# Performance work log

Hardware: AMD Instinct MI355X
Metric: run time of the kernel (lower is better)

The kernel has to match this reference:

```python
import jax, jax.numpy as jnp
import numpy as np

N, C, E, Q, H, NC = 50000, 128, 1600000, 500000, 256, 2
BN_EPS = 1e-5


def gru_step(x, h, wih, whh, bih, bhh):
    # single-step torch.nn.GRU, gate order (r, z, n); x,h: [C, C] rows as batch
    gi = x @ wih.T + bih
    gh = h @ whh.T + bhh
    ir, iz, inn = jnp.split(gi, 3, axis=-1)
    hr, hz, hn = jnp.split(gh, 3, axis=-1)
    r = jax.nn.sigmoid(ir + hr)
    z = jax.nn.sigmoid(iz + hz)
    n = jnp.tanh(inn + r * hn)
    return (1.0 - z) * n + z * h


def gcn_conv(x, w, src, dst, ew):
    # GCNConv with fixed weight w and symmetric gcn_norm incl. self-loops
    xw = x @ w
    deg = jnp.zeros((N,), xw.dtype).at[dst].add(ew) + 1.0  # +1 self-loop
    dinv = jax.lax.rsqrt(deg)
    norm = dinv[src] * ew * dinv[dst]
    out = jnp.zeros_like(xw).at[dst].add(xw[src] * norm[:, None])
    return out + xw * (dinv * dinv)[:, None]  # self-loop contribution


def evolve_gcno(x, src, dst, ew, w_init, wih, whh, bih, bhh):
    w = gru_step(w_init, w_init, wih, whh, bih, bhh)
    return gcn_conv(x, w, src, dst, ew)


def setup_inputs():
    key = jax.random.key(0)
    ks = jax.random.split(key, 40)
    inp = {}
    inp["X"] = jax.random.normal(ks[0], (N, C), jnp.float32)
    inp["edge_index"] = jax.random.randint(ks[1], (2, E), 0, N, jnp.int32)
    inp["edge_weight"] = jax.random.uniform(ks[2], (E,), jnp.float32)
    inp["edge1"] = jax.random.randint(ks[3], (Q,), 0, N, jnp.int32)
    inp["edge2"] = jax.random.randint(ks[4], (Q,), 0, N, jnp.int32)
    s = 1.0 / np.sqrt(C)
    i = 5
    for l in range(2):
        inp[f"w{l}_init"] = jax.random.uniform(ks[i], (C, C), jnp.float32, -s, s); i += 1
        inp[f"w{l}_ih"] = jax.random.uniform(ks[i], (3 * C, C), jnp.float32, -s, s); i += 1
        inp[f"w{l}_hh"] = jax.random.uniform(ks[i], (3 * C, C), jnp.float32, -s, s); i += 1
        inp[f"b{l}_ih"] = jax.random.uniform(ks[i], (3 * C,), jnp.float32, -s, s); i += 1
        inp[f"b{l}_hh"] = jax.random.uniform(ks[i], (3 * C,), jnp.float32, -s, s); i += 1
    dims = [(H, C), (H, H), (NC, H)]
    for l, (o, fi) in enumerate(dims):
        sl = 1.0 / np.sqrt(fi)
        inp[f"lin_w{l}"] = jax.random.uniform(ks[i], (o, fi), jnp.float32, -sl, sl); i += 1
        inp[f"lin_b{l}"] = jax.random.uniform(ks[i], (o,), jnp.float32, -sl, sl); i += 1
    for l in range(2):
        inp[f"bn_g{l}"] = jax.random.uniform(ks[i], (H,), jnp.float32, 0.5, 1.5); i += 1
        inp[f"bn_b{l}"] = 0.1 * jax.random.normal(ks[i], (H,), jnp.float32); i += 1
        inp[f"bn_m{l}"] = 0.1 * jax.random.normal(ks[i], (H,), jnp.float32); i += 1
        inp[f"bn_v{l}"] = jax.random.uniform(ks[i], (H,), jnp.float32, 0.5, 1.5); i += 1
    return inp


def reference(X, edge_index, edge_weight, edge1, edge2,
              w0_init, w0_ih, w0_hh, b0_ih, b0_hh,
              w1_init, w1_ih, w1_hh, b1_ih, b1_hh,
              lin_w0, lin_b0, lin_w1, lin_b1, lin_w2, lin_b2,
              bn_g0, bn_b0, bn_m0, bn_v0, bn_g1, bn_b1, bn_m1, bn_v1):
    src, dst = edge_index[0], edge_index[1]
    # EGCNO: two EvolveGCNO layers + relu (dropout is identity in eval)
    x = jax.nn.relu(evolve_gcno(X, src, dst, edge_weight, w0_init, w0_ih, w0_hh, b0_ih, b0_hh))
    x = jax.nn.relu(evolve_gcno(x, src, dst, edge_weight, w1_init, w1_ih, w1_hh, b1_ih, b1_hh))
    # edge pair gather + hadamard
    h = x[edge1] * x[edge2]  # [Q, C]
    bn = [(bn_g0, bn_b0, bn_m0, bn_v0), (bn_g1, bn_b1, bn_m1, bn_v1)]
    lins = [(lin_w0, lin_b0), (lin_w1, lin_b1)]
    for (w, b), (g, bb, m, v) in zip(lins, bn):
        h = h @ w.T + b
        h = g * (h - m) * jax.lax.rsqrt(v + BN_EPS) + bb  # BatchNorm1d (eval)
        h = jax.nn.relu(h)
    h = h @ lin_w2.T + lin_b2
    return jax.nn.log_softmax(h, axis=-1)
```

## Files before the change

### kernel.cpp

```cpp
#include <hip/hip_runtime.h>
#include <math.h>

#define N_NODES 50000
#define C_DIM   128
#define E_EDGES 1600000
#define Q_PAIRS 500000
#define H_DIM   256
#define N_CLS   2
#define BN_EPS  1e-5f

typedef __attribute__((ext_vector_type(8))) short bf16x8;
typedef __attribute__((ext_vector_type(4))) short s16x4;
typedef __attribute__((ext_vector_type(4))) unsigned short u16x4;
typedef __attribute__((ext_vector_type(4))) float f32x4;

#define VMCNT0 asm volatile("s_waitcnt vmcnt(0)" ::: "memory")
#define VMCNT1 asm volatile("s_waitcnt vmcnt(1)" ::: "memory")
#define VMCNT2 asm volatile("s_waitcnt vmcnt(2)" ::: "memory")
#define SBAR do { __builtin_amdgcn_s_barrier(); \
                  __builtin_amdgcn_sched_barrier(0); } while (0)

#define DEG_SCALE 2097152.0f

__device__ __forceinline__ unsigned short f2bf(float x) {
    unsigned u = __float_as_uint(x);
    u += 0x7fffu + ((u >> 16) & 1u);
    return (unsigned short)(u >> 16);
}
__device__ __forceinline__ float bf2f(unsigned short h) {
    return __uint_as_float(((unsigned)h) << 16);
}

__global__ __launch_bounds__(256) void k_init(unsigned long long* dpack, int* qcnt) {
    int i = blockIdx.x * 256 + threadIdx.x;
    if (i < N_NODES) { dpack[i] = 0ULL; qcnt[i] = 0; }
}
__global__ __launch_bounds__(256) void k_deg_hist(const int* __restrict__ dst,
                                                  const float* __restrict__ ew,
                                                  unsigned long long* dpack) {
    int e = blockIdx.x * 256 + threadIdx.x;
    if (e < E_EDGES) {
        unsigned pv = __float2uint_rn(ew[e] * DEG_SCALE);
        atomicAdd(&dpack[dst[e]], (1ULL << 32) | (unsigned long long)pv);
    }
}
__global__ __launch_bounds__(256) void k_qhist(const int* __restrict__ e1, int* qcnt) {
    int q = blockIdx.x * 256 + threadIdx.x;
    if (q < Q_PAIRS) atomicAdd(&qcnt[e1[q]], 1);
}

__global__ __launch_bounds__(1024) void k_scan1(const int* __restrict__ cnt, int stride,
                                                int* __restrict__ locincl,
                                                int* __restrict__ bsum) {
    __shared__ int pa[1024], pb[1024];
    int t = threadIdx.x;
    int x = blockIdx.x * 1024 + t;
    int v = (x < N_NODES) ? cnt[(size_t)x * stride] : 0;
    pa[t] = v;
    __syncthreads();
    int* sp = pa; int* dp = pb;
    for (int o = 1; o < 1024; o <<= 1) {
        int u = sp[t] + ((t >= o) ? sp[t - o] : 0);
        dp[t] = u;
        __syncthreads();
        int* tmp = sp; sp = dp; dp = tmp;
    }
    if (x < N_NODES) locincl[x] = sp[t];
    if (t == 1023) bsum[blockIdx.x] = sp[1023];
}
__global__ __launch_bounds__(64) void k_scan2(const int* __restrict__ bsum,
                                              int* __restrict__ boff) {
    int t = threadIdx.x;
    int v = (t < 49) ? bsum[t] : 0;
    int own = v;
    for (int o = 1; o < 64; o <<= 1) {
        int u = __shfl_up(v, o, 64);
        if (t >= o) v += u;
    }
    if (t < 49) boff[t] = v - own;
}
__global__ __launch_bounds__(1024) void k_scan3(const int* __restrict__ cnt, int stride,
                                                int* __restrict__ pos,
                                                const int* __restrict__ boff,
                                                int* __restrict__ off,
                                                const unsigned long long* __restrict__ dpack,
                                                float* __restrict__ dinv) {
    int x = blockIdx.x * 1024 + threadIdx.x;
    if (x >= N_NODES) return;
    int incl = pos[x];
    int c = cnt[(size_t)x * stride];
    int o = boff[blockIdx.x] + incl - c;
    off[x] = o;
    pos[x] = o;
    if (x == N_NODES - 1) off[N_NODES] = o + c;
    if (dpack) {
        unsigned lo = (unsigned)(dpack[x] & 0xffffffffULL);
        dinv[x] = rsqrtf(1.0f + (float)lo * (1.0f / DEG_SCALE));
    }
}

__global__ __launch_bounds__(256) void k_fill(const int* __restrict__ src,
                                              const int* __restrict__ dst,
                                              const float* __restrict__ ew,
                                              const float* __restrict__ dinv,
                                              int* pos,
                                              int2* __restrict__ csr) {
    int e = blockIdx.x * 256 + threadIdx.x;
    if (e >= E_EDGES) return;
    int s = src[e], d = dst[e];
    int slot = atomicAdd(&pos[d], 1);
    int2 p;
    p.x = s;
    p.y = __float_as_int(dinv[s] * ew[e] * dinv[d]);
    csr[slot] = p;
}
__global__ __launch_bounds__(256) void k_qfill(const int* __restrict__ e1,
                                               const int* __restrict__ e2,
                                               int* qpos,
                                               int2* __restrict__ qpair,
                                               int* __restrict__ qidx) {
    int q = blockIdx.x * 256 + threadIdx.x;
    if (q >= Q_PAIRS) return;
    int a = e1[q];
    int slot = atomicAdd(&qpos[a], 1);
    int2 p; p.x = a; p.y = e2[q];
    qpair[slot] = p;
    qidx[slot] = q;
}

__global__ __launch_bounds__(128) void k_gru2(
    const float* __restrict__ wi0, const float* __restrict__ wih0, const float* __restrict__ whh0,
    const float* __restrict__ bih0, const float* __restrict__ bhh0, float* __restrict__ we0,
    const float* __restrict__ wi1, const float* __restrict__ wih1, const float* __restrict__ whh1,
    const float* __restrict__ bih1, const float* __restrict__ bhh1, float* __restrict__ we1) {
    __shared__ float xrow[C_DIM];
    int layer = blockIdx.x >> 7;
    int i = blockIdx.x & 127, j = threadIdx.x;
    const float* w_init = layer ? wi1 : wi0;
    const float* wih = layer ? wih1 : wih0;
    const float* whh = layer ? whh1 : whh0;
    const float* bih = layer ? bih1 : bih0;
    const float* bhh = layer ? bhh1 : bhh0;
    float* w_out = layer ? we1 : we0;
    xrow[j] = w_init[i * C_DIM + j];
    __syncthreads();
    float gi[3], gh[3];
#pragma unroll
    for (int g = 0; g < 3; ++g) {
        const float* wi = wih + (size_t)(g * C_DIM + j) * C_DIM;
        const float* wh = whh + (size_t)(g * C_DIM + j) * C_DIM;
        float ai = 0.f, ah = 0.f;
        for (int k = 0; k < C_DIM; ++k) { ai += xrow[k] * wi[k]; ah += xrow[k] * wh[k]; }
        gi[g] = ai + bih[g * C_DIM + j];
        gh[g] = ah + bhh[g * C_DIM + j];
    }
    float r = 1.f / (1.f + expf(-(gi[0] + gh[0])));
    float z = 1.f / (1.f + expf(-(gi[1] + gh[1])));
    float n = tanhf(gi[2] + r * gh[2]);
    w_out[i * C_DIM + j] = (1.f - z) * n + z * xrow[j];
}

__global__ __launch_bounds__(256) void k_xbf(const float* __restrict__ x,
                                             unsigned short* __restrict__ xb) {
    int i = (blockIdx.x * 256 + threadIdx.x) * 8;
    f32x4 a = *(const f32x4*)(x + i);
    f32x4 b = *(const f32x4*)(x + i + 4);
    bf16x8 o;
#pragma unroll
    for (int e = 0; e < 4; ++e) { o[e] = (short)f2bf(a[e]); o[e + 4] = (short)f2bf(b[e]); }
    *(bf16x8*)(xb + i) = o;
}

__global__ __launch_bounds__(256) void k_agg(const unsigned short* __restrict__ xb,
                                             const float* __restrict__ dinv,
                                             const int* __restrict__ off,
                                             const int2* __restrict__ csr,
                                             float* __restrict__ agg) {
    int tid = blockIdx.x * 256 + threadIdx.x;
    int n = tid >> 5;
    int c = (tid & 31) << 2;
    float dv = dinv[n];
    float d2 = dv * dv;
    u16x4 xs = *(const u16x4*)(xb + (size_t)n * C_DIM + c);
    float4 acc;
    acc.x = d2 * bf2f(xs[0]); acc.y = d2 * bf2f(xs[1]);
    acc.z = d2 * bf2f(xs[2]); acc.w = d2 * bf2f(xs[3]);
    int i = off[n], e = off[n + 1];
    for (; i + 8 <= e; i += 8) {
        int2 q0 = csr[i], q1 = csr[i + 1], q2 = csr[i + 2], q3 = csr[i + 3];
        int2 q4 = csr[i + 4], q5 = csr[i + 5], q6 = csr[i + 6], q7 = csr[i + 7];
        u16x4 v0 = *(const u16x4*)(xb + (size_t)q0.x * C_DIM + c);
        u16x4 v1 = *(const u16x4*)(xb + (size_t)q1.x * C_DIM + c);
        u16x4 v2 = *(const u16x4*)(xb + (size_t)q2.x * C_DIM + c);
        u16x4 v3 = *(const u16x4*)(xb + (size_t)q3.x * C_DIM + c);
        u16x4 v4 = *(const u16x4*)(xb + (size_t)q4.x * C_DIM + c);
        u16x4 v5 = *(const u16x4*)(xb + (size_t)q5.x * C_DIM + c);
        u16x4 v6 = *(const u16x4*)(xb + (size_t)q6.x * C_DIM + c);
        u16x4 v7 = *(const u16x4*)(xb + (size_t)q7.x * C_DIM + c);
        float w0 = __int_as_float(q0.y), w1 = __int_as_float(q1.y);
        float w2 = __int_as_float(q2.y), w3 = __int_as_float(q3.y);
        float w4 = __int_as_float(q4.y), w5 = __int_as_float(q5.y);
        float w6 = __int_as_float(q6.y), w7 = __int_as_float(q7.y);
        acc.x += w0 * bf2f(v0[0]) + w1 * bf2f(v1[0]) + w2 * bf2f(v2[0]) + w3 * bf2f(v3[0])
               + w4 * bf2f(v4[0]) + w5 * bf2f(v5[0]) + w6 * bf2f(v6[0]) + w7 * bf2f(v7[0]);
        acc.y += w0 * bf2f(v0[1]) + w1 * bf2f(v1[1]) + w2 * bf2f(v2[1]) + w3 * bf2f(v3[1])
               + w4 * bf2f(v4[1]) + w5 * bf2f(v5[1]) + w6 * bf2f(v6[1]) + w7 * bf2f(v7[1]);
        acc.z += w0 * bf2f(v0[2]) + w1 * bf2f(v1[2]) + w2 * bf2f(v2[2]) + w3 * bf2f(v3[2])
               + w4 * bf2f(v4[2]) + w5 * bf2f(v5[2]) + w6 * bf2f(v6[2]) + w7 * bf2f(v7[2]);
        acc.w += w0 * bf2f(v0[3]) + w1 * bf2f(v1[3]) + w2 * bf2f(v2[3]) + w3 * bf2f(v3[3])
               + w4 * bf2f(v4[3]) + w5 * bf2f(v5[3]) + w6 * bf2f(v6[3]) + w7 * bf2f(v7[3]);
    }
    for (; i < e; ++i) {
        int2 pe = csr[i];
        float w = __int_as_float(pe.y);
        u16x4 v = *(const u16x4*)(xb + (size_t)pe.x * C_DIM + c);
        acc.x += w * bf2f(v[0]); acc.y += w * bf2f(v[1]);
        acc.z += w * bf2f(v[2]); acc.w += w * bf2f(v[3]);
    }
    *(float4*)(agg + (size_t)n * C_DIM + c) = acc;
}

__global__ __launch_bounds__(256) void k_prep_w(const float* __restrict__ w,
                                                const float* __restrict__ g,
                                                const float* __restrict__ v,
                                                int kdim, int total,
                                                unsigned short* __restrict__ outp) {
    int idx = blockIdx.x * 256 + threadIdx.x;
    if (idx >= total) return;
    int e = idx & 7, col = (idx >> 3) & 255, kg = (idx >> 11) & 3;
    int kb = idx >> 13;
    int k = kb * 32 + kg * 8 + e;
    float sc = g[col] * rsqrtf(v[col] + BN_EPS);
    outp[idx] = f2bf(w[(size_t)col * kdim + k] * sc);
}
__global__ __launch_bounds__(256) void k_prep_conv(const float* __restrict__ we0,
                                                   const float* __restrict__ we1,
                                                   unsigned short* __restrict__ Wc0,
                                                   unsigned short* __restrict__ Wc1) {
    int idx = blockIdx.x * 256 + threadIdx.x;
    int e = idx & 7, col = (idx >> 3) & 127, kg = (idx >> 10) & 3;
    int plane = (idx >> 12) & 1, kb = (idx >> 13) & 3, layer = idx >> 15;
    int k = kb * 32 + kg * 8 + e;
    const float* we = layer ? we1 : we0;
    float x = we[(size_t)k * C_DIM + col];
    unsigned short hi = f2bf(x);
    unsigned short o = plane ? f2bf(x - bf2f(hi)) : hi;
    (layer ? Wc1 : Wc0)[idx & 32767] = o;
}

__global__ __launch_bounds__(512) void k_prep_shift(
    const float* __restrict__ lb0, const float* __restrict__ bg0, const float* __restrict__ bb0,
    const float* __restrict__ bm0, const float* __restrict__ bv0,
    const float* __restrict__ lb1, const float* __restrict__ bg1, const float* __restrict__ bb1,
    const float* __restrict__ bm1, const float* __restrict__ bv1,
    float* __restrict__ shift0, float* __restrict__ shift1) {
    int j = threadIdx.x;
    if (j < 256) {
        float sc = bg0[j] * rsqrtf(bv0[j] + BN_EPS);
        shift0[j] = (lb0[j] - bm0[j]) * sc + bb0[j];
    } else {
        int i = j - 256;
        float sc = bg1[i] * rsqrtf(bv1[i] + BN_EPS);
        shift1[i] = (lb1[i] - bm1[i]) * sc + bb1[i];
    }
}

template <int OUT_BF>
__global__ __launch_bounds__(512) void k_gemm(const float* __restrict__ agg,
                                              const unsigned short* __restrict__ Wc,
                                              float* __restrict__ y,
                                              unsigned short* __restrict__ yb) {
    __shared__ __align__(16) char smem[3 * 8192];
    const int t = threadIdx.x, lane = t & 63, wave = t >> 6;
    const int qg = wave >> 1, ch = wave & 1;
    const int l16 = lane & 15, kg = lane >> 4;
    const int qrow = qg * 16 + l16;
    const int node = blockIdx.x * 64 + qrow;
    const int nodec = node < N_NODES ? node : N_NODES - 1;

    auto STG = [&](int sidx, int b) {
        const char* g = (const char*)Wc + sidx * 8192 + wave * 1024 + lane * 16;
        char* d = smem + b * 8192 + wave * 1024;
        __builtin_amdgcn_global_load_lds((const __attribute__((address_space(1))) void*)g,
                                         (__attribute__((address_space(3))) void*)d, 16, 0, 0);
    };
    STG(0, 0); STG(1, 1);

    bf16x8 bh[4], bl[4];
    const float* ar = agg + (size_t)nodec * C_DIM;
#pragma unroll
    for (int kb = 0; kb < 4; ++kb) {
        int k0 = kb * 32 + kg * 8;
        f32x4 a0 = *(const f32x4*)(ar + k0);
        f32x4 a1 = *(const f32x4*)(ar + k0 + 4);
#pragma unroll
        for (int e = 0; e < 4; ++e) {
            unsigned short h0 = f2bf(a0[e]);
            bh[kb][e] = (short)h0; bl[kb][e] = (short)f2bf(a0[e] - bf2f(h0));
            unsigned short h1 = f2bf(a1[e]);
            bh[kb][e + 4] = (short)h1; bl[kb][e + 4] = (short)f2bf(a1[e] - bf2f(h1));
        }
    }
    f32x4 acc[4];
#pragma unroll
    for (int i = 0; i < 4; ++i) acc[i] = 0.f;

#pragma unroll
    for (int s = 0; s < 8; ++s) {
        if (s < 7) { VMCNT1; } else { VMCNT0; }
        SBAR;
        if (s + 2 < 8) STG(s + 2, (s + 2) % 3);
        const unsigned short* strip = (const unsigned short*)(smem + (s % 3) * 8192);
        const int kb = s >> 1;
        __builtin_amdgcn_s_setprio(1);
#pragma unroll
        for (int jc8 = 0; jc8 < 4; ++jc8) {
            int col = (ch * 4 + jc8) * 16 + l16;
            bf16x8 a = *(const bf16x8*)&strip[kg * 1024 + col * 8];
            acc[jc8] = __builtin_amdgcn_mfma_f32_16x16x32_bf16(a, bh[kb], acc[jc8], 0, 0, 0);
            if ((s & 1) == 0)
                acc[jc8] = __builtin_amdgcn_mfma_f32_16x16x32_bf16(a, bl[kb], acc[jc8], 0, 0, 0);
        }
        __builtin_amdgcn_s_setprio(0);
    }

    if (node < N_NODES) {
#pragma unroll
        for (int jc8 = 0; jc8 < 4; ++jc8) {
            int j0 = (ch * 4 + jc8) * 16 + kg * 4;
            if (OUT_BF) {
                u16x4 v;
#pragma unroll
                for (int r = 0; r < 4; ++r) v[r] = f2bf(fmaxf(acc[jc8][r], 0.f));
                *(u16x4*)(yb + (size_t)node * C_DIM + j0) = v;
            } else {
                float4 v;
                v.x = fmaxf(acc[jc8][0], 0.f); v.y = fmaxf(acc[jc8][1], 0.f);
                v.z = fmaxf(acc[jc8][2], 0.f); v.w = fmaxf(acc[jc8][3], 0.f);
                *(float4*)(y + (size_t)node * C_DIM + j0) = v;
            }
        }
    }
}

__global__ __launch_bounds__(512, 4) void k_mlp(const float* __restrict__ y,
                                             const int2* __restrict__ qpair,
                                             const int* __restrict__ qidx,
                                             const unsigned short* __restrict__ W0p,
                                             const unsigned short* __restrict__ W1p,
                                             const float* __restrict__ shift0,
                                             const float* __restrict__ shift1,
                                             const float* __restrict__ w2,
                                             const float* __restrict__ b2,
                                             float* __restrict__ out) {
    __shared__ __align__(16) char smem[81920];
    unsigned short* l1b = (unsigned short*)(smem + 49152);
    float* red = (float*)smem;

    const int t = threadIdx.x;
    const int lane = t & 63;
    const int wave = t >> 6;
    const int qs = wave >> 2, cg = wave & 3;
    const int l16 = lane & 15, kg = lane >> 4;
    const int qb = blockIdx.x * 64;

    auto STG = [&](const unsigned short* W, int sidx, int b) {
        const char* g = (const char*)W + ((size_t)sidx << 14) + wave * 2048 + lane * 16;
        char* d = smem + b * 16384 + wave * 2048;
        __builtin_amdgcn_global_load_lds((const __attribute__((address_space(1))) void*)g,
                                         (__attribute__((address_space(3))) void*)d, 16, 0, 0);
        __builtin_amdgcn_global_load_lds((const __attribute__((address_space(1))) void*)(g + 1024),
                                         (__attribute__((address_space(3))) void*)(d + 1024), 16, 0, 0);
    };

    STG(W0p, 0, 0); STG(W0p, 1, 1);

    {
        int k2 = lane * 2;
        int G = lane >> 2;
        int off = k2 & 7;
#pragma unroll
        for (int qi = 0; qi < 8; ++qi) {
            int qrow = wave * 8 + qi;
            int q = qb + qrow; if (q >= Q_PAIRS) q = Q_PAIRS - 1;
            int2 pr = qpair[q];
            const float* ya = y + (size_t)pr.x * C_DIM;
            const float* yb = y + (size_t)pr.y * C_DIM;
            float2 a = *(const float2*)(ya + k2);
            float2 b = *(const float2*)(yb + k2);
            int idx = qrow * 256 + ((G ^ (qrow & 7)) << 3) + off;
            l1b[idx] = f2bf(a.x * b.x);
            l1b[idx + 1] = f2bf(a.y * b.y);
        }
    }
    __syncthreads();

    bf16x8 bh[2][4];
#pragma unroll
    for (int qq = 0; qq < 2; ++qq) {
        int qrow = qs * 32 + qq * 16 + l16;
#pragma unroll
        for (int kb = 0; kb < 4; ++kb) {
            int gidx = qrow * 256 + (((kb * 4 + kg) ^ (qrow & 7)) * 8);
            bh[qq][kb] = *(const bf16x8*)&l1b[gidx];
        }
    }

    f32x4 acc[2][4];
#pragma unroll
    for (int qq = 0; qq < 2; ++qq)
#pragma unroll
        for (int jc = 0; jc < 4; ++jc) acc[qq][jc] = 0.f;

#pragma unroll
    for (int s = 0; s < 4; ++s) {
        if (s < 3) { VMCNT2; } else { VMCNT0; }
        SBAR;
        if (s + 2 < 4) STG(W0p, s + 2, (s + 2) % 3);
        const unsigned short* strip = (const unsigned short*)(smem + (s % 3) * 16384);
        __builtin_amdgcn_s_setprio(1);
#pragma unroll
        for (int jc = 0; jc < 4; ++jc) {
            int col = cg * 64 + jc * 16 + l16;
            bf16x8 a = *(const bf16x8*)&strip[kg * 2048 + col * 8];
            acc[0][jc] = __builtin_amdgcn_mfma_f32_16x16x32_bf16(a, bh[0][s], acc[0][jc], 0, 0, 0);
            acc[1][jc] = __builtin_amdgcn_mfma_f32_16x16x32_bf16(a, bh[1][s], acc[1][jc], 0, 0, 0);
        }
        __builtin_amdgcn_s_setprio(0);
    }

#pragma unroll
    for (int qq = 0; qq < 2; ++qq) {
        int qrow = qs * 32 + qq * 16 + l16;
#pragma unroll
        for (int jc = 0; jc < 4; ++jc) {
            int jg = cg * 4 + jc;
            int j0 = jg * 16 + kg * 4;
            f32x4 sh = *(const f32x4*)(shift0 + j0);
            s16x4 th;
#pragma unroll
            for (int r = 0; r < 4; ++r)
                th[r] = (short)f2bf(fmaxf(acc[qq][jc][r] + sh[r], 0.f));
            int G = jg * 2 + (kg >> 1);
            int idx = qrow * 256 + ((G ^ (qrow & 7)) * 8) + (kg & 1) * 4;
            *(s16x4*)&l1b[idx] = th;
        }
    }
    __syncthreads();

    f32x4 acc2[2][4];
#pragma unroll
    for (int qq = 0; qq < 2; ++qq)
#pragma unroll
        for (int jc = 0; jc < 4; ++jc) acc2[qq][jc] = 0.f;
    STG(W1p, 0, 0); STG(W1p, 1, 1);
    bf16x8 bh2[2];
#pragma unroll
    for (int s = 0; s < 8; ++s) {
        if (s < 7) { VMCNT2; } else { VMCNT0; }
        SBAR;
        if (s + 2 < 8) STG(W1p, s + 2, (s + 2) % 3);
        const unsigned short* strip = (const unsigned short*)(smem + (s % 3) * 16384);
#pragma unroll
        for (int qq = 0; qq < 2; ++qq) {
            int qrow = qs * 32 + qq * 16 + l16;
            int gidx = qrow * 256 + (((s * 4 + kg) ^ (qrow & 7)) * 8);
            bh2[qq] = *(const bf16x8*)&l1b[gidx];
        }
        __builtin_amdgcn_s_setprio(1);
#pragma unroll
        for (int jc = 0; jc < 4; ++jc) {
            int col = cg * 64 + jc * 16 + l16;
            bf16x8 a = *(const bf16x8*)&strip[kg * 2048 + col * 8];
            acc2[0][jc] = __builtin_amdgcn_mfma_f32_16x16x32_bf16(a, bh2[0], acc2[0][jc], 0, 0, 0);
            acc2[1][jc] = __builtin_amdgcn_mfma_f32_16x16x32_bf16(a, bh2[1], acc2[1][jc], 0, 0, 0);
        }
        __builtin_amdgcn_s_setprio(0);
    }

    float p[2][2] = {};
#pragma unroll
    for (int qq = 0; qq < 2; ++qq)
#pragma unroll
        for (int jc = 0; jc < 4; ++jc) {
            int j0 = (cg * 4 + jc) * 16 + kg * 4;
            f32x4 sh = *(const f32x4*)(shift1 + j0);
            f32x4 wa = *(const f32x4*)(w2 + j0);
            f32x4 wb = *(const f32x4*)(w2 + H_DIM + j0);
#pragma unroll
            for (int r = 0; r < 4; ++r) {
                float v = fmaxf(acc2[qq][jc][r] + sh[r], 0.f);
                p[qq][0] += v * wa[r];
                p[qq][1] += v * wb[r];
            }
        }
#pragma unroll
    for (int qq = 0; qq < 2; ++qq) {
        p[qq][0] += __shfl_xor(p[qq][0], 16, 64); p[qq][0] += __shfl_xor(p[qq][0], 32, 64);
        p[qq][1] += __shfl_xor(p[qq][1], 16, 64); p[qq][1] += __shfl_xor(p[qq][1], 32, 64);
    }
    __syncthreads();
    if (kg == 0) {
#pragma unroll
        for (int qq = 0; qq < 2; ++qq) {
            int base = ((qs * 2 + qq) * 16 + l16) * 2;
            red[(base + 0) * 4 + cg] = p[qq][0];
            red[(base + 1) * 4 + cg] = p[qq][1];
        }
    }
    __syncthreads();
    if (t < 64) {
        int q = qb + t;
        if (q < Q_PAIRS) {
            int base = t * 2;
            float l0 = red[base * 4 + 0] + red[base * 4 + 1] + red[base * 4 + 2] + red[base * 4 + 3] + b2[0];
            float l1v = red[(base + 1) * 4 + 0] + red[(base + 1) * 4 + 1]
                      + red[(base + 1) * 4 + 2] + red[(base + 1) * 4 + 3] + b2[1];
            float mx = fmaxf(l0, l1v);
            float lse = mx + logf(expf(l0 - mx) + expf(l1v - mx));
            float2 o; o.x = l0 - lse; o.y = l1v - lse;
            *(float2*)(out + (size_t)qidx[q] * N_CLS) = o;
        }
    }
}

extern "C" void kernel_launch(void* const* d_in, const int* in_sizes, int n_in,
                              void* d_out, int out_size, void* d_ws, size_t ws_size,
                              hipStream_t stream) {
    const float* X  = (const float*)d_in[0];
    const int*   ei = (const int*)d_in[1];
    const float* ew = (const float*)d_in[2];
    const int*   e1 = (const int*)d_in[3];
    const int*   e2 = (const int*)d_in[4];
    const float* w_init[2] = {(const float*)d_in[5],  (const float*)d_in[10]};
    const float* w_ih[2]   = {(const float*)d_in[6],  (const float*)d_in[11]};
    const float* w_hh[2]   = {(const float*)d_in[7],  (const float*)d_in[12]};
    const float* b_ih[2]   = {(const float*)d_in[8],  (const float*)d_in[13]};
    const float* b_hh[2]   = {(const float*)d_in[9],  (const float*)d_in[14]};
    const float* lw0 = (const float*)d_in[15]; const float* lb0 = (const float*)d_in[16];
    const float* lw1 = (const float*)d_in[17]; const float* lb1 = (const float*)d_in[18];
    const float* lw2 = (const float*)d_in[19]; const float* lb2 = (const float*)d_in[20];
    const float* bg0 = (const float*)d_in[21]; const float* bb0 = (const float*)d_in[22];
    const float* bm0 = (const float*)d_in[23]; const float* bv0 = (const float*)d_in[24];
    const float* bg1 = (const float*)d_in[25]; const float* bb1 = (const float*)d_in[26];
    const float* bm1 = (const float*)d_in[27]; const float* bv1 = (const float*)d_in[28];
    const int* src = ei;
    const int* dst = ei + E_EDGES;

    char* ws = (char*)d_ws;
    size_t o = 0;
    auto alloc = [&](size_t bytes) { char* p = ws + o; o += (bytes + 63) & ~(size_t)63; return p; };
    float* bufA   = (float*)alloc((size_t)N_NODES * C_DIM * 4);
    float* bufB   = (float*)alloc((size_t)N_NODES * C_DIM * 4);
    unsigned short* xbf = (unsigned short*)alloc((size_t)N_NODES * C_DIM * 2);
    unsigned short* ybf = (unsigned short*)alloc((size_t)N_NODES * C_DIM * 2);
    float* dinv   = (float*)alloc(N_NODES * 4);
    float* we0    = (float*)alloc(C_DIM * C_DIM * 4);
    float* we1    = (float*)alloc(C_DIM * C_DIM * 4);
    float* shift0 = (float*)alloc(H_DIM * 4);
    float* shift1 = (float*)alloc(H_DIM * 4);
    unsigned long long* dpack = (unsigned long long*)alloc((size_t)N_NODES * 8);
    int*   pos    = (int*)alloc(N_NODES * 4);
    int*   off    = (int*)alloc((N_NODES + 1) * 4);
    int*   bsum   = (int*)alloc(64 * 4);
    int*   boff   = (int*)alloc(64 * 4);
    int*   qcnt   = (int*)alloc(N_NODES * 4);
    int*   qpos   = (int*)alloc(N_NODES * 4);
    int*   qoff   = (int*)alloc((N_NODES + 1) * 4);
    int*   qbsum  = (int*)alloc(64 * 4);
    int*   qboff  = (int*)alloc(64 * 4);
    int2*  csr    = (int2*)alloc((size_t)E_EDGES * 8);
    int2*  qpair  = (int2*)alloc((size_t)Q_PAIRS * 8);
    int*   qidx   = (int*)alloc((size_t)Q_PAIRS * 4);
    unsigned short* W0p = (unsigned short*)alloc(32768 * 2);
    unsigned short* W1p = (unsigned short*)alloc(65536 * 2);
    unsigned short* Wc0 = (unsigned short*)alloc(32768 * 2);
    unsigned short* Wc1 = (unsigned short*)alloc(32768 * 2);
    if (o > ws_size) return;

    dim3 b256(256);
    const int gN = (N_NODES + 255) / 256;
    const int gE = (E_EDGES + 255) / 256;
    const int gQ = (Q_PAIRS + 255) / 256;

    k_init<<<gN, b256, 0, stream>>>(dpack, qcnt);
    k_deg_hist<<<gE, b256, 0, stream>>>(dst, ew, dpack);
    k_qhist<<<gQ, b256, 0, stream>>>(e1, qcnt);
    k_scan1<<<49, dim3(1024), 0, stream>>>((const int*)dpack + 1, 2, pos, bsum);
    k_scan2<<<1, dim3(64), 0, stream>>>(bsum, boff);
    k_scan3<<<49, dim3(1024), 0, stream>>>((const int*)dpack + 1, 2, pos, boff, off, dpack, dinv);
    k_fill<<<gE, b256, 0, stream>>>(src, dst, ew, dinv, pos, csr);
    k_scan1<<<49, dim3(1024), 0, stream>>>(qcnt, 1, qpos, qbsum);
    k_scan2<<<1, dim3(64), 0, stream>>>(qbsum, qboff);
    k_scan3<<<49, dim3(1024), 0, stream>>>(qcnt, 1, qpos, qboff, qoff, nullptr, nullptr);
    k_qfill<<<gQ, b256, 0, stream>>>(e1, e2, qpos, qpair, qidx);

    k_gru2<<<256, dim3(128), 0, stream>>>(w_init[0], w_ih[0], w_hh[0], b_ih[0], b_hh[0], we0,
                                          w_init[1], w_ih[1], w_hh[1], b_ih[1], b_hh[1], we1);
    k_prep_conv<<<256, b256, 0, stream>>>(we0, we1, Wc0, Wc1);
    k_prep_w<<<128, b256, 0, stream>>>(lw0, bg0, bv0, C_DIM, 32768, W0p);
    k_prep_w<<<256, b256, 0, stream>>>(lw1, bg1, bv1, H_DIM, 65536, W1p);
    k_prep_shift<<<1, dim3(512), 0, stream>>>(lb0, bg0, bb0, bm0, bv0, lb1, bg1, bb1, bm1, bv1, shift0, shift1);
    k_xbf<<<(N_NODES * C_DIM) / 2048, b256, 0, stream>>>(X, xbf);

    const int ga = (N_NODES * 32) / 256;
    const int gg = (N_NODES + 63) / 64;
    k_agg<<<ga, b256, 0, stream>>>(xbf, dinv, off, csr, bufA);
    k_gemm<1><<<gg, dim3(512), 0, stream>>>(bufA, Wc0, bufB, ybf);
    k_agg<<<ga, b256, 0, stream>>>(ybf, dinv, off, csr, bufA);
    k_gemm<0><<<gg, dim3(512), 0, stream>>>(bufA, Wc1, bufB, ybf);
    k_mlp<<<(Q_PAIRS + 63) / 64, dim3(512), 0, stream>>>(bufB, qpair, qidx, W0p, W1p,
                                                         shift0, shift1, lw2, lb2, (float*)d_out);
}
```

Measured before the change: 572.9 us.

## Merge preprocessing kernels into fewer launches and widen aggregation vectors

Launches that do the same job for the edge and query pair streams are merged into single kernels that branch on block index. The affected stages are histogram, three-pass scan and fill, plus GRU with bf16 cast and the weight prep kernels, and a memset replaces the init kernel. This cuts launch count and lets the independent edge and query work run at the same time. The aggregation kernel now has each thread handle 8 bf16 channels with 16-byte loads instead of 4, which halves the thread count and raises per-thread register use.

Measured after the change: 584.0 us. No clear change (+1.9%).

```diff
diff --git a/kernel.cpp b/kernel.cpp
--- a/kernel.cpp
+++ b/kernel.cpp
@@ -9,6 +9,9 @@
 #define N_CLS   2
 #define BN_EPS  1e-5f
 
+#define GE_BLK  6250
+#define GQ_BLK  1954
+
 typedef __attribute__((ext_vector_type(8))) short bf16x8;
 typedef __attribute__((ext_vector_type(4))) short s16x4;
 typedef __attribute__((ext_vector_type(4))) unsigned short u16x4;
@@ -31,31 +34,34 @@
     return __uint_as_float(((unsigned)h) << 16);
 }
 
-__global__ __launch_bounds__(256) void k_init(unsigned long long* dpack, int* qcnt) {
-    int i = blockIdx.x * 256 + threadIdx.x;
-    if (i < N_NODES) { dpack[i] = 0ULL; qcnt[i] = 0; }
-}
-__global__ __launch_bounds__(256) void k_deg_hist(const int* __restrict__ dst,
-                                                  const float* __restrict__ ew,
-                                                  unsigned long long* dpack) {
-    int e = blockIdx.x * 256 + threadIdx.x;
-    if (e < E_EDGES) {
-        unsigned pv = __float2uint_rn(ew[e] * DEG_SCALE);
-        atomicAdd(&dpack[dst[e]], (1ULL << 32) | (unsigned long long)pv);
-    }
-}
-__global__ __launch_bounds__(256) void k_qhist(const int* __restrict__ e1, int* qcnt) {
-    int q = blockIdx.x * 256 + threadIdx.x;
-    if (q < Q_PAIRS) atomicAdd(&qcnt[e1[q]], 1);
-}
-
-__global__ __launch_bounds__(1024) void k_scan1(const int* __restrict__ cnt, int stride,
-                                                int* __restrict__ locincl,
-                                                int* __restrict__ bsum) {
+__global__ __launch_bounds__(256) void k_hist2(const int* __restrict__ dst,
+                                               const float* __restrict__ ew,
+                                               unsigned long long* dpack,
+                                               const int* __restrict__ e1,
+                                               int* qcnt) {
+    int b = blockIdx.x;
+    if (b < GE_BLK) {
+        int e = b * 256 + threadIdx.x;
+        if (e < E_EDGES) {
+            unsigned pv = __float2uint_rn(ew[e] * DEG_SCALE);
+            atomicAdd(&dpack[dst[e]], (1ULL << 32) | (unsigned long long)pv);
+        }
+    } else {
+        int q = (b - GE_BLK) * 256 + threadIdx.x;
+        if (q < Q_PAIRS) atomicAdd(&qcnt[e1[q]], 1);
+    }
+}
+
+__global__ __launch_bounds__(1024) void k_scan1f(const unsigned long long* __restrict__ dpack,
+                                                 const int* __restrict__ qcnt,
+                                                 int* __restrict__ pos, int* __restrict__ qpos,
+                                                 int* __restrict__ bsum) {
     __shared__ int pa[1024], pb[1024];
+    int seg = blockIdx.x / 49, blk = blockIdx.x % 49;
     int t = threadIdx.x;
-    int x = blockIdx.x * 1024 + t;
-    int v = (x < N_NODES) ? cnt[(size_t)x * stride] : 0;
+    int x = blk * 1024 + t;
+    int v = 0;
+    if (x < N_NODES) v = seg ? qcnt[x] : (int)(dpack[x] >> 32);
     pa[t] = v;
     __syncthreads();
     int* sp = pa; int* dp = pb;
@@ -65,110 +71,167 @@
         __syncthreads();
         int* tmp = sp; sp = dp; dp = tmp;
     }
-    if (x < N_NODES) locincl[x] = sp[t];
-    if (t == 1023) bsum[blockIdx.x] = sp[1023];
-}
-__global__ __launch_bounds__(64) void k_scan2(const int* __restrict__ bsum,
-                                              int* __restrict__ boff) {
+    if (x < N_NODES) (seg ? qpos : pos)[x] = sp[t];
+    if (t == 1023) bsum[seg * 64 + blk] = sp[1023];
+}
+__global__ __launch_bounds__(128) void k_scan2f(const int* __restrict__ bsum,
+                                                int* __restrict__ boff) {
     int t = threadIdx.x;
-    int v = (t < 49) ? bsum[t] : 0;
+    int seg = t >> 6, lane = t & 63;
+    int v = (lane < 49) ? bsum[seg * 64 + lane] : 0;
     int own = v;
     for (int o = 1; o < 64; o <<= 1) {
         int u = __shfl_up(v, o, 64);
-        if (t >= o) v += u;
-    }
-    if (t < 49) boff[t] = v - own;
-}
-__global__ __launch_bounds__(1024) void k_scan3(const int* __restrict__ cnt, int stride,
-                                                int* __restrict__ pos,
-                                                const int* __restrict__ boff,
-                                                int* __restrict__ off,
-                                                const unsigned long long* __restrict__ dpack,
-                                                float* __restrict__ dinv) {
-    int x = blockIdx.x * 1024 + threadIdx.x;
+        if (lane >= o) v += u;
+    }
+    if (lane < 49) boff[seg * 64 + lane] = v - own;
+}
+__global__ __launch_bounds__(1024) void k_scan3f(const unsigned long long* __restrict__ dpack,
+                                                 const int* __restrict__ qcnt,
+                                                 int* __restrict__ pos, int* __restrict__ qpos,
+                                                 const int* __restrict__ boff,
+                                                 int* __restrict__ off, int* __restrict__ qoff,
+                                                 float* __restrict__ dinv) {
+    int seg = blockIdx.x / 49, blk = blockIdx.x % 49;
+    int x = blk * 1024 + threadIdx.x;
     if (x >= N_NODES) return;
-    int incl = pos[x];
-    int c = cnt[(size_t)x * stride];
-    int o = boff[blockIdx.x] + incl - c;
-    off[x] = o;
-    pos[x] = o;
-    if (x == N_NODES - 1) off[N_NODES] = o + c;
-    if (dpack) {
+    int c = seg ? qcnt[x] : (int)(dpack[x] >> 32);
+    int* ppos = seg ? qpos : pos;
+    int* poff = seg ? qoff : off;
+    int incl = ppos[x];
+    int o = boff[seg * 64 + blk] + incl - c;
+    poff[x] = o;
+    ppos[x] = o;
+    if (x == N_NODES - 1) poff[N_NODES] = o + c;
+    if (!seg) {
         unsigned lo = (unsigned)(dpack[x] & 0xffffffffULL);
         dinv[x] = rsqrtf(1.0f + (float)lo * (1.0f / DEG_SCALE));
     }
 }
 
-__global__ __launch_bounds__(256) void k_fill(const int* __restrict__ src,
-                                              const int* __restrict__ dst,
-                                              const float* __restrict__ ew,
-                                              const float* __restrict__ dinv,
-                                              int* pos,
-                                              int2* __restrict__ csr) {
-    int e = blockIdx.x * 256 + threadIdx.x;
-    if (e >= E_EDGES) return;
-    int s = src[e], d = dst[e];
-    int slot = atomicAdd(&pos[d], 1);
-    int2 p;
-    p.x = s;
-    p.y = __float_as_int(dinv[s] * ew[e] * dinv[d]);
-    csr[slot] = p;
-}
-__global__ __launch_bounds__(256) void k_qfill(const int* __restrict__ e1,
+__global__ __launch_bounds__(256) void k_fill2(const int* __restrict__ src,
+                                               const int* __restrict__ dst,
+                                               const float* __restrict__ ew,
+                                               const float* __restrict__ dinv,
+                                               int* pos, int2* __restrict__ csr,
+                                               const int* __restrict__ e1,
                                                const int* __restrict__ e2,
-                                               int* qpos,
-                                               int2* __restrict__ qpair,
+                                               int* qpos, int2* __restrict__ qpair,
                                                int* __restrict__ qidx) {
-    int q = blockIdx.x * 256 + threadIdx.x;
-    if (q >= Q_PAIRS) return;
-    int a = e1[q];
-    int slot = atomicAdd(&qpos[a], 1);
-    int2 p; p.x = a; p.y = e2[q];
-    qpair[slot] = p;
-    qidx[slot] = q;
-}
-
-__global__ __launch_bounds__(128) void k_gru2(
+    int b = blockIdx.x;
+    if (b < GE_BLK) {
+        int e = b * 256 + threadIdx.x;
+        if (e < E_EDGES) {
+            int s = src[e], d = dst[e];
+            int slot = atomicAdd(&pos[d], 1);
+            int2 p;
+            p.x = s;
+            p.y = __float_as_int(dinv[s] * ew[e] * dinv[d]);
+            csr[slot] = p;
+        }
+    } else {
+        int q = (b - GE_BLK) * 256 + threadIdx.x;
+        if (q < Q_PAIRS) {
+            int a = e1[q];
+            int slot = atomicAdd(&qpos[a], 1);
+            int2 p; p.x = a; p.y = e2[q];
+            qpair[slot] = p;
+            qidx[slot] = q;
+        }
+    }
+}
+
+__global__ __launch_bounds__(256) void k_gru_xbf(
     const float* __restrict__ wi0, const float* __restrict__ wih0, const float* __restrict__ whh0,
     const float* __restrict__ bih0, const float* __restrict__ bhh0, float* __restrict__ we0,
     const float* __restrict__ wi1, const float* __restrict__ wih1, const float* __restrict__ whh1,
-    const float* __restrict__ bih1, const float* __restrict__ bhh1, float* __restrict__ we1) {
-    __shared__ float xrow[C_DIM];
-    int layer = blockIdx.x >> 7;
-    int i = blockIdx.x & 127, j = threadIdx.x;
-    const float* w_init = layer ? wi1 : wi0;
-    const float* wih = layer ? wih1 : wih0;
-    const float* whh = layer ? whh1 : whh0;
-    const float* bih = layer ? bih1 : bih0;
-    const float* bhh = layer ? bhh1 : bhh0;
-    float* w_out = layer ? we1 : we0;
-    xrow[j] = w_init[i * C_DIM + j];
-    __syncthreads();
-    float gi[3], gh[3];
-#pragma unroll
-    for (int g = 0; g < 3; ++g) {
-        const float* wi = wih + (size_t)(g * C_DIM + j) * C_DIM;
-        const float* wh = whh + (size_t)(g * C_DIM + j) * C_DIM;
-        float ai = 0.f, ah = 0.f;
-        for (int k = 0; k < C_DIM; ++k) { ai += xrow[k] * wi[k]; ah += xrow[k] * wh[k]; }
-        gi[g] = ai + bih[g * C_DIM + j];
-        gh[g] = ah + bhh[g * C_DIM + j];
-    }
-    float r = 1.f / (1.f + expf(-(gi[0] + gh[0])));
-    float z = 1.f / (1.f + expf(-(gi[1] + gh[1])));
-    float n = tanhf(gi[2] + r * gh[2]);
-    w_out[i * C_DIM + j] = (1.f - z) * n + z * xrow[j];
-}
-
-__global__ __launch_bounds__(256) void k_xbf(const float* __restrict__ x,
-                                             unsigned short* __restrict__ xb) {
-    int i = (blockIdx.x * 256 + threadIdx.x) * 8;
-    f32x4 a = *(const f32x4*)(x + i);
-    f32x4 b = *(const f32x4*)(x + i + 4);
-    bf16x8 o;
-#pragma unroll
-    for (int e = 0; e < 4; ++e) { o[e] = (short)f2bf(a[e]); o[e + 4] = (short)f2bf(b[e]); }
-    *(bf16x8*)(xb + i) = o;
+    const float* __restrict__ bih1, const float* __restrict__ bhh1, float* __restrict__ we1,
+    const float* __restrict__ x, unsigned short* __restrict__ xb) {
+    if (blockIdx.x < 256) {
+        __shared__ float xrow[C_DIM];
+        int layer = blockIdx.x >> 7;
+        int i = blockIdx.x & 127, j = threadIdx.x;
+        const float* w_init = layer ? wi1 : wi0;
+        const float* wih = layer ? wih1 : wih0;
+        const float* whh = layer ? whh1 : whh0;
+        const float* bih = layer ? bih1 : bih0;
+        const float* bhh = layer ? bhh1 : bhh0;
+        float* w_out = layer ? we1 : we0;
+        if (j < C_DIM) xrow[j] = w_init[i * C_DIM + j];
+        __syncthreads();
+        if (j < C_DIM) {
+            float gi[3], gh[3];
+#pragma unroll
+            for (int g = 0; g < 3; ++g) {
+                const float* wi = wih + (size_t)(g * C_DIM + j) * C_DIM;
+                const float* wh = whh + (size_t)(g * C_DIM + j) * C_DIM;
+                float ai = 0.f, ah = 0.f;
+                for (int k = 0; k < C_DIM; ++k) { ai += xrow[k] * wi[k]; ah += xrow[k] * wh[k]; }
+                gi[g] = ai + bih[g * C_DIM + j];
+                gh[g] = ah + bhh[g * C_DIM + j];
+            }
+            float r = 1.f / (1.f + expf(-(gi[0] + gh[0])));
+            float z = 1.f / (1.f + expf(-(gi[1] + gh[1])));
+            float n = tanhf(gi[2] + r * gh[2]);
+            w_out[i * C_DIM + j] = (1.f - z) * n + z * xrow[j];
+        }
+    } else {
+        int i = ((blockIdx.x - 256) * 256 + threadIdx.x) * 8;
+        f32x4 a = *(const f32x4*)(x + i);
+        f32x4 b = *(const f32x4*)(x + i + 4);
+        bf16x8 o;
+#pragma unroll
+        for (int e = 0; e < 4; ++e) { o[e] = (short)f2bf(a[e]); o[e + 4] = (short)f2bf(b[e]); }
+        *(bf16x8*)(xb + i) = o;
+    }
+}
+
+__global__ __launch_bounds__(256) void k_prep_all(
+    const float* __restrict__ we0, const float* __restrict__ we1,
+    unsigned short* __restrict__ Wc0, unsigned short* __restrict__ Wc1,
+    const float* __restrict__ lw0, const float* __restrict__ lw1,
+    unsigned short* __restrict__ W0p, unsigned short* __restrict__ W1p,
+    const float* __restrict__ lb0, const float* __restrict__ bg0, const float* __restrict__ bb0,
+    const float* __restrict__ bm0, const float* __restrict__ bv0,
+    const float* __restrict__ lb1, const float* __restrict__ bg1, const float* __restrict__ bb1,
+    const float* __restrict__ bm1, const float* __restrict__ bv1,
+    float* __restrict__ shift0, float* __restrict__ shift1) {
+    int b = blockIdx.x, t = threadIdx.x;
+    if (b < 256) {
+        int idx = b * 256 + t;
+        int e = idx & 7, col = (idx >> 3) & 127, kg = (idx >> 10) & 3;
+        int plane = (idx >> 12) & 1, kb = (idx >> 13) & 3, layer = idx >> 15;
+        int k = kb * 32 + kg * 8 + e;
+        const float* we = layer ? we1 : we0;
+        float x = we[(size_t)k * C_DIM + col];
+        unsigned short hi = f2bf(x);
+        unsigned short o = plane ? f2bf(x - bf2f(hi)) : hi;
+        (layer ? Wc1 : Wc0)[idx & 32767] = o;
+    } else if (b < 384) {
+        int idx = (b - 256) * 256 + t;
+        int e = idx & 7, col = (idx >> 3) & 255, kg = (idx >> 11) & 3;
+        int kb = idx >> 13;
+        int k = kb * 32 + kg * 8 + e;
+        float sc = bg0[col] * rsqrtf(bv0[col] + BN_EPS);
+        W0p[idx] = f2bf(lw0[(size_t)col * C_DIM + k] * sc);
+    } else if (b < 640) {
+        int idx = (b - 384) * 256 + t;
+        int e = idx & 7, col = (idx >> 3) & 255, kg = (idx >> 11) & 3;
+        int kb = idx >> 13;
+        int k = kb * 32 + kg * 8 + e;
+        float sc = bg1[col] * rsqrtf(bv1[col] + BN_EPS);
+        W1p[idx] = f2bf(lw1[(size_t)col * H_DIM + k] * sc);
+    } else {
+        int j = (b - 640) * 256 + t;
+        if (j < 256) {
+            float sc = bg0[j] * rsqrtf(bv0[j] + BN_EPS);
+            shift0[j] = (lb0[j] - bm0[j]) * sc + bb0[j];
+        } else {
+            int i = j - 256;
+            float sc = bg1[i] * rsqrtf(bv1[i] + BN_EPS);
+            shift1[i] = (lb1[i] - bm1[i]) * sc + bb1[i];
+        }
+    }
 }
 
 __global__ __launch_bounds__(256) void k_agg(const unsigned short* __restrict__ xb,
@@ -177,92 +240,50 @@
                                              const int2* __restrict__ csr,
                                              float* __restrict__ agg) {
     int tid = blockIdx.x * 256 + threadIdx.x;
-    int n = tid >> 5;
-    int c = (tid & 31) << 2;
+    int n = tid >> 4;
+    int c = (tid & 15) << 3;
     float dv = dinv[n];
     float d2 = dv * dv;
-    u16x4 xs = *(const u16x4*)(xb + (size_t)n * C_DIM + c);
-    float4 acc;
-    acc.x = d2 * bf2f(xs[0]); acc.y = d2 * bf2f(xs[1]);
-    acc.z = d2 * bf2f(xs[2]); acc.w = d2 * bf2f(xs[3]);
-    int i = off[n], e = off[n + 1];
-    for (; i + 8 <= e; i += 8) {
+    bf16x8 xs = *(const bf16x8*)(xb + (size_t)n * C_DIM + c);
+    float acc[8];
+#pragma unroll
+    for (int e = 0; e < 8; ++e) acc[e] = d2 * bf2f((unsigned short)xs[e]);
+    int i = off[n], en = off[n + 1];
+    for (; i + 8 <= en; i += 8) {
         int2 q0 = csr[i], q1 = csr[i + 1], q2 = csr[i + 2], q3 = csr[i + 3];
         int2 q4 = csr[i + 4], q5 = csr[i + 5], q6 = csr[i + 6], q7 = csr[i + 7];
-        u16x4 v0 = *(const u16x4*)(xb + (size_t)q0.x * C_DIM + c);
-        u16x4 v1 = *(const u16x4*)(xb + (size_t)q1.x * C_DIM + c);
-        u16x4 v2 = *(const u16x4*)(xb + (size_t)q2.x * C_DIM + c);
-        u16x4 v3 = *(const u16x4*)(xb + (size_t)q3.x * C_DIM + c);
-        u16x4 v4 = *(const u16x4*)(xb + (size_t)q4.x * C_DIM + c);
-        u16x4 v5 = *(const u16x4*)(xb + (size_t)q5.x * C_DIM + c);
-        u16x4 v6 = *(const u16x4*)(xb + (size_t)q6.x * C_DIM + c);
-        u16x4 v7 = *(const u16x4*)(xb + (size_t)q7.x * C_DIM + c);
+        bf16x8 v0 = *(const bf16x8*)(xb + (size_t)q0.x * C_DIM + c);
+        bf16x8 v1 = *(const bf16x8*)(xb + (size_t)q1.x * C_DIM + c);
+        bf16x8 v2 = *(const bf16x8*)(xb + (size_t)q2.x * C_DIM + c);
+        bf16x8 v3 = *(const bf16x8*)(xb + (size_t)q3.x * C_DIM + c);
+        bf16x8 v4 = *(const bf16x8*)(xb + (size_t)q4.x * C_DIM + c);
+        bf16x8 v5 = *(const bf16x8*)(xb + (size_t)q5.x * C_DIM + c);
+        bf16x8 v6 = *(const bf16x8*)(xb + (size_t)q6.x * C_DIM + c);
+        bf16x8 v7 = *(const bf16x8*)(xb + (size_t)q7.x * C_DIM + c);
         float w0 = __int_as_float(q0.y), w1 = __int_as_float(q1.y);
         float w2 = __int_as_float(q2.y), w3 = __int_as_float(q3.y);
         float w4 = __int_as_float(q4.y), w5 = __int_as_float(q5.y);
         float w6 = __int_as_float(q6.y), w7 = __int_as_float(q7.y);
-        acc.x += w0 * bf2f(v0[0]) + w1 * bf2f(v1[0]) + w2 * bf2f(v2[0]) + w3 * bf2f(v3[0])
-               + w4 * bf2f(v4[0]) + w5 * bf2f(v5[0]) + w6 * bf2f(v6[0]) + w7 * bf2f(v7[0]);
-        acc.y += w0 * bf2f(v0[1]) + w1 * bf2f(v1[1]) + w2 * bf2f(v2[1]) + w3 * bf2f(v3[1])
-               + w4 * bf2f(v4[1]) + w5 * bf2f(v5[1]) + w6 * bf2f(v6[1]) + w7 * bf2f(v7[1]);
-        acc.z += w0 * bf2f(v0[2]) + w1 * bf2f(v1[2]) + w2 * bf2f(v2[2]) + w3 * bf2f(v3[2])
-               + w4 * bf2f(v4[2]) + w5 * bf2f(v5[2]) + w6 * bf2f(v6[2]) + w7 * bf2f(v7[2]);
-        acc.w += w0 * bf2f(v0[3]) + w1 * bf2f(v1[3]) + w2 * bf2f(v2[3]) + w3 * bf2f(v3[3])
-               + w4 * bf2f(v4[3]) + w5 * bf2f(v5[3]) + w6 * bf2f(v6[3]) + w7 * bf2f(v7[3]);
-    }
-    for (; i < e; ++i) {
+#pragma unroll
+        for (int e = 0; e < 8; ++e) {
+            acc[e] += w0 * bf2f((unsigned short)v0[e]) + w1 * bf2f((unsigned short)v1[e])
+                    + w2 * bf2f((unsigned short)v2[e]) + w3 * bf2f((unsigned short)v3[e])
+                    + w4 * bf2f((unsigned short)v4[e]) + w5 * bf2f((unsigned short)v5[e])
+                    + w6 * bf2f((unsigned short)v6[e]) + w7 * bf2f((unsigned short)v7[e]);
+        }
+    }
+    for (; i < en; ++i) {
         int2 pe = csr[i];
         float w = __int_as_float(pe.y);
-        u16x4 v = *(const u16x4*)(xb + (size_t)pe.x * C_DIM + c);
-        acc.x += w * bf2f(v[0]); acc.y += w * bf2f(v[1]);
-        acc.z += w * bf2f(v[2]); acc.w += w * bf2f(v[3]);
-    }
-    *(float4*)(agg + (size_t)n * C_DIM + c) = acc;
-}
-
-__global__ __launch_bounds__(256) void k_prep_w(const float* __restrict__ w,
-                                                const float* __restrict__ g,
-                                                const float* __restrict__ v,
-                                                int kdim, int total,
-                                                unsigned short* __restrict__ outp) {
-    int idx = blockIdx.x * 256 + threadIdx.x;
-    if (idx >= total) return;
-    int e = idx & 7, col = (idx >> 3) & 255, kg = (idx >> 11) & 3;
-    int kb = idx >> 13;
-    int k = kb * 32 + kg * 8 + e;
-    float sc = g[col] * rsqrtf(v[col] + BN_EPS);
-    outp[idx] = f2bf(w[(size_t)col * kdim + k] * sc);
-}
-__global__ __launch_bounds__(256) void k_prep_conv(const float* __restrict__ we0,
-                                                   const float* __restrict__ we1,
-                                                   unsigned short* __restrict__ Wc0,
-                                                   unsigned short* __restrict__ Wc1) {
-    int idx = blockIdx.x * 256 + threadIdx.x;
-    int e = idx & 7, col = (idx >> 3) & 127, kg = (idx >> 10) & 3;
-    int plane = (idx >> 12) & 1, kb = (idx >> 13) & 3, layer = idx >> 15;
-    int k = kb * 32 + kg * 8 + e;
-    const float* we = layer ? we1 : we0;
-    float x = we[(size_t)k * C_DIM + col];
-    unsigned short hi = f2bf(x);
-    unsigned short o = plane ? f2bf(x - bf2f(hi)) : hi;
-    (layer ? Wc1 : Wc0)[idx & 32767] = o;
-}
-
-__global__ __launch_bounds__(512) void k_prep_shift(
-    const float* __restrict__ lb0, const float* __restrict__ bg0, const float* __restrict__ bb0,
-    const float* __restrict__ bm0, const float* __restrict__ bv0,
-    const float* __restrict__ lb1, const float* __restrict__ bg1, const float* __restrict__ bb1,
-    const float* __restrict__ bm1, const float* __restrict__ bv1,
-    float* __restrict__ shift0, float* __restrict__ shift1) {
-    int j = threadIdx.x;
-    if (j < 256) {
-        float sc = bg0[j] * rsqrtf(bv0[j] + BN_EPS);
-        shift0[j] = (lb0[j] - bm0[j]) * sc + bb0[j];
-    } else {
-        int i = j - 256;
-        float sc = bg1[i] * rsqrtf(bv1[i] + BN_EPS);
-        shift1[i] = (lb1[i] - bm1[i]) * sc + bb1[i];
-    }
+        bf16x8 v = *(const bf16x8*)(xb + (size_t)pe.x * C_DIM + c);
+#pragma unroll
+        for (int e = 0; e < 8; ++e) acc[e] += w * bf2f((unsigned short)v[e]);
+    }
+    float4 o0, o1;
+    o0.x = acc[0]; o0.y = acc[1]; o0.z = acc[2]; o0.w = acc[3];
+    o1.x = acc[4]; o1.y = acc[5]; o1.z = acc[6]; o1.w = acc[7];
+    *(float4*)(agg + (size_t)n * C_DIM + c) = o0;
+    *(float4*)(agg + (size_t)n * C_DIM + c + 4) = o1;
 }
 
 template <int OUT_BF>
@@ -554,21 +575,19 @@
     float* bufB   = (float*)alloc((size_t)N_NODES * C_DIM * 4);
     unsigned short* xbf = (unsigned short*)alloc((size_t)N_NODES * C_DIM * 2);
     unsigned short* ybf = (unsigned short*)alloc((size_t)N_NODES * C_DIM * 2);
+    unsigned long long* dpack = (unsigned long long*)alloc((size_t)N_NODES * 8);
+    int*   qcnt   = (int*)alloc(N_NODES * 4);
     float* dinv   = (float*)alloc(N_NODES * 4);
     float* we0    = (float*)alloc(C_DIM * C_DIM * 4);
     float* we1    = (float*)alloc(C_DIM * C_DIM * 4);
     float* shift0 = (float*)alloc(H_DIM * 4);
     float* shift1 = (float*)alloc(H_DIM * 4);
-    unsigned long long* dpack = (unsigned long long*)alloc((size_t)N_NODES * 8);
     int*   pos    = (int*)alloc(N_NODES * 4);
     int*   off    = (int*)alloc((N_NODES + 1) * 4);
-    int*   bsum   = (int*)alloc(64 * 4);
-    int*   boff   = (int*)alloc(64 * 4);
-    int*   qcnt   = (int*)alloc(N_NODES * 4);
     int*   qpos   = (int*)alloc(N_NODES * 4);
     int*   qoff   = (int*)alloc((N_NODES + 1) * 4);
-    int*   qbsum  = (int*)alloc(64 * 4);
-    int*   qboff  = (int*)alloc(64 * 4);
+    int*   bsum   = (int*)alloc(128 * 4);
+    int*   boff   = (int*)alloc(128 * 4);
     int2*  csr    = (int2*)alloc((size_t)E_EDGES * 8);
     int2*  qpair  = (int2*)alloc((size_t)Q_PAIRS * 8);
     int*   qidx   = (int*)alloc((size_t)Q_PAIRS * 4);
@@ -579,31 +598,23 @@
     if (o > ws_size) return;
 
     dim3 b256(256);
-    const int gN = (N_NODES + 255) / 256;
-    const int gE = (E_EDGES + 255) / 256;
-    const int gQ = (Q_PAIRS + 255) / 256;
-
-    k_init<<<gN, b256, 0, stream>>>(dpack, qcnt);
-    k_deg_hist<<<gE, b256, 0, stream>>>(dst, ew, dpack);
-    k_qhist<<<gQ, b256, 0, stream>>>(e1, qcnt);
-    k_scan1<<<49, dim3(1024), 0, stream>>>((const int*)dpack + 1, 2, pos, bsum);
-    k_scan2<<<1, dim3(64), 0, stream>>>(bsum, boff);
-    k_scan3<<<49, dim3(1024), 0, stream>>>((const int*)dpack + 1, 2, pos, boff, off, dpack, dinv);
-    k_fill<<<gE, b256, 0, stream>>>(src, dst, ew, dinv, pos, csr);
-    k_scan1<<<49, dim3(1024), 0, stream>>>(qcnt, 1, qpos, qbsum);
-    k_scan2<<<1, dim3(64), 0, stream>>>(qbsum, qboff);
-    k_scan3<<<49, dim3(1024), 0, stream>>>(qcnt, 1, qpos, qboff, qoff, nullptr, nullptr);
-    k_qfill<<<gQ, b256, 0, stream>>>(e1, e2, qpos, qpair, qidx);
-
-    k_gru2<<<256, dim3(128), 0, stream>>>(w_init[0], w_ih[0], w_hh[0], b_ih[0], b_hh[0], we0,
-                                          w_init[1], w_ih[1], w_hh[1], b_ih[1], b_hh[1], we1);
-    k_prep_conv<<<256, b256, 0, stream>>>(we0, we1, Wc0, Wc1);
-    k_prep_w<<<128, b256, 0, stream>>>(lw0, bg0, bv0, C_DIM, 32768, W0p);
-    k_prep_w<<<256, b256, 0, stream>>>(lw1, bg1, bv1, H_DIM, 65536, W1p);
-    k_prep_shift<<<1, dim3(512), 0, stream>>>(lb0, bg0, bb0, bm0, bv0, lb1, bg1, bb1, bm1, bv1, shift0, shift1);
-    k_xbf<<<(N_NODES * C_DIM) / 2048, b256, 0, stream>>>(X, xbf);
-
-    const int ga = (N_NODES * 32) / 256;
+
+    hipMemsetAsync(dpack, 0, (size_t)N_NODES * 8 + (size_t)N_NODES * 4, stream);
+    k_hist2<<<GE_BLK + GQ_BLK, b256, 0, stream>>>(dst, ew, dpack, e1, qcnt);
+    k_scan1f<<<98, dim3(1024), 0, stream>>>(dpack, qcnt, pos, qpos, bsum);
+    k_scan2f<<<1, dim3(128), 0, stream>>>(bsum, boff);
+    k_scan3f<<<98, dim3(1024), 0, stream>>>(dpack, qcnt, pos, qpos, boff, off, qoff, dinv);
+    k_fill2<<<GE_BLK + GQ_BLK, b256, 0, stream>>>(src, dst, ew, dinv, pos, csr,
+                                                  e1, e2, qpos, qpair, qidx);
+
+    k_gru_xbf<<<256 + 3125, b256, 0, stream>>>(w_init[0], w_ih[0], w_hh[0], b_ih[0], b_hh[0], we0,
+                                               w_init[1], w_ih[1], w_hh[1], b_ih[1], b_hh[1], we1,
+                                               X, xbf);
+    k_prep_all<<<642, b256, 0, stream>>>(we0, we1, Wc0, Wc1, lw0, lw1, W0p, W1p,
+                                         lb0, bg0, bb0, bm0, bv0,
+                                         lb1, bg1, bb1, bm1, bv1, shift0, shift1);
+
+    const int ga = (N_NODES * 16) / 256;
     const int gg = (N_NODES + 63) / 64;
     k_agg<<<ga, b256, 0, stream>>>(xbf, dinv, off, csr, bufA);
     k_gemm<1><<<gg, dim3(512), 0, stream>>>(bufA, Wc0, bufB, ybf);
```
